# Kernel tuning notes

Measured on AMD Instinct MI355X. Metric: run time of the kernel, lower is better.

The kernel has to match this reference:

```python
import jax, jax.numpy as jnp
import numpy as np
import math

B, S, HID, H = 2, 1024, 768, 12
D = HID // H  # 64
ALPHA = 32.0


def setup_inputs() -> dict:
    key = jax.random.key(0)
    ks = jax.random.split(key, 8)
    return {
        "hidden_states": jax.random.normal(ks[0], (B, S, HID), jnp.float32),
        "attention_mask": jnp.zeros((B, 1, 1, S), jnp.float32),
        "head_mask": jnp.ones((1, H, 1, 1), jnp.float32),
        "rel_pos": jax.random.normal(ks[1], (B, H, S, S), jnp.float32),
        "rel_2d_pos": jax.random.normal(ks[2], (B, H, S, S), jnp.float32),
        "Wq": jax.random.normal(ks[3], (HID, HID), jnp.float32) * 0.02,
        "bq": jnp.zeros((HID,), jnp.float32),
        "Wk": jax.random.normal(ks[4], (HID, HID), jnp.float32) * 0.02,
        "bk": jnp.zeros((HID,), jnp.float32),
        "Wv": jax.random.normal(ks[5], (HID, HID), jnp.float32) * 0.02,
        "bv": jnp.zeros((HID,), jnp.float32),
    }


def _heads(x):
    # [B,S,HID] -> [B,H,S,D]
    return x.reshape(B, S, H, D).transpose(0, 2, 1, 3)


def cogview_softmax(scores, alpha=ALPHA):
    s = scores / alpha
    m = jnp.max(s, axis=-1, keepdims=True)
    return jax.nn.softmax((s - m) * alpha, axis=-1)


def reference(hidden_states, attention_mask, head_mask, rel_pos, rel_2d_pos,
              Wq, bq, Wk, bk, Wv, bv):
    norm = math.sqrt(D)
    q = _heads(hidden_states @ Wq + bq) / norm   # [B,H,S,D]
    k = _heads(hidden_states @ Wk + bk)
    v = _heads(hidden_states @ Wv + bv)
    scores = jnp.einsum("bhsd,bhtd->bhst", q, k)
    scores = scores + (rel_pos + rel_2d_pos) / norm
    scores = scores + attention_mask
    probs = cogview_softmax(scores)              # [B,H,S,S]
    probs = probs * head_mask
    ctx = jnp.einsum("bhst,bhtd->bhsd", probs, v)
    ctx = ctx.transpose(0, 2, 1, 3).reshape(B, S, HID)
    return ctx
```

## Files before the change

kernel.cpp:

```cpp
#include <hip/hip_runtime.h>
#include <hip/hip_bf16.h>
#include <cstdint>

#define BB   2
#define SS   1024
#define HIDD 768
#define NH   12
#define DH   64
#define BH   (BB*NH)

typedef short bf16x8 __attribute__((ext_vector_type(8)));
typedef float f32x4  __attribute__((ext_vector_type(4)));

__device__ __forceinline__ unsigned short f2b(float x) {
    union { float f; uint32_t u; } v; v.f = x;
    uint32_t u = v.u;
    uint32_t r = (u + 0x7fffu + ((u >> 16) & 1u)) >> 16;
    return (unsigned short)r;
}

__device__ __forceinline__ void async16(const void* g, void* l) {
    __builtin_amdgcn_global_load_lds(
        (const __attribute__((address_space(1))) unsigned int*)g,
        (__attribute__((address_space(3))) unsigned int*)l,
        16, 0, 0);
}

__global__ void cvt_x(const float* __restrict__ x, unsigned short* __restrict__ xb) {
    int i = blockIdx.x * blockDim.x + threadIdx.x;
    float4 v = ((const float4*)x)[i];
    ushort4 o;
    o.x = f2b(v.x); o.y = f2b(v.y); o.z = f2b(v.z); o.w = f2b(v.w);
    ((ushort4*)xb)[i] = o;
}

__global__ void transpose_w(const float* __restrict__ Wq, const float* __restrict__ Wk,
                            const float* __restrict__ Wv, unsigned short* __restrict__ Wt) {
    __shared__ float tile[32][33];
    const int w = blockIdx.z;
    const float* W = (w == 0) ? Wq : (w == 1) ? Wk : Wv;
    const int tx = threadIdx.x & 31, ty = threadIdx.x >> 5;
    const int k0 = blockIdx.x * 32, n0 = blockIdx.y * 32;
    for (int p = 0; p < 4; ++p)
        tile[ty + p * 8][tx] = W[(k0 + ty + p * 8) * HIDD + n0 + tx];
    __syncthreads();
    for (int p = 0; p < 4; ++p) {
        int n = n0 + ty + p * 8;
        Wt[(w * HIDD + n) * HIDD + k0 + tx] = f2b(tile[tx][ty + p * 8]);
    }
}

__global__ __launch_bounds__(256) void qkv_gemm(
    const unsigned short* __restrict__ Xb, const unsigned short* __restrict__ Wt,
    const float* __restrict__ bq, const float* __restrict__ bk, const float* __restrict__ bv,
    unsigned short* __restrict__ Qh, unsigned short* __restrict__ Kh,
    unsigned short* __restrict__ Vh) {
    __shared__ __align__(16) unsigned short lA[2][128 * 32];
    __shared__ __align__(16) unsigned short lB[2][64 * 32];
    const int t = threadIdx.x;
    const int wave = t >> 6, lane = t & 63;
    const int l15 = lane & 15, quad = lane >> 4;
    const int m0 = blockIdx.x * 128;
    const int n0 = blockIdx.y * 64;
    const int wm = wave * 32;

    f32x4 acc[2][4] = {};

    auto stage = [&](int k0, int b) {
        #pragma unroll
        for (int r = 0; r < 2; ++r) {
            int ci = r * 256 + t;
            async16(Xb + (m0 + (ci >> 2)) * HIDD + k0 + (ci & 3) * 8,
                    &lA[b][(r * 256 + wave * 64) * 8]);
        }
        async16(Wt + (n0 + (t >> 2)) * HIDD + k0 + (t & 3) * 8,
                &lB[b][(wave * 64) * 8]);
    };

    stage(0, 0);
    for (int ki = 0; ki < 24; ++ki) {
        const int cur = ki & 1;
        __syncthreads();
        if (ki < 23) stage((ki + 1) * 32, cur ^ 1);
        bf16x8 af[2], bf[4];
        #pragma unroll
        for (int i = 0; i < 2; ++i)
            af[i] = *(const bf16x8*)&lA[cur][(wm + i * 16 + l15) * 32 + quad * 8];
        #pragma unroll
        for (int j = 0; j < 4; ++j)
            bf[j] = *(const bf16x8*)&lB[cur][(j * 16 + l15) * 32 + quad * 8];
        #pragma unroll
        for (int i = 0; i < 2; ++i)
            #pragma unroll
            for (int j = 0; j < 4; ++j)
                acc[i][j] = __builtin_amdgcn_mfma_f32_16x16x32_bf16(af[i], bf[j], acc[i][j], 0, 0, 0);
    }

    const int sect = (n0 >= 1536) ? 2 : (n0 >= 768) ? 1 : 0;
    const float* bias = (sect == 0) ? bq : (sect == 1) ? bk : bv;
    unsigned short* dst = (sect == 0) ? Qh : (sect == 1) ? Kh : Vh;
    const float scale = (sect == 0) ? 0.125f : 1.0f;
    #pragma unroll
    for (int i = 0; i < 2; ++i) {
        #pragma unroll
        for (int j = 0; j < 4; ++j) {
            int n  = n0 + j * 16 + l15;
            int nn = n - sect * HIDD;
            int h = nn >> 6, d = nn & 63;
            float bval = bias[nn];
            #pragma unroll
            for (int r = 0; r < 4; ++r) {
                int m = m0 + wm + i * 16 + quad * 4 + r;
                int b = m >> 10, s = m & 1023;
                float v = (acc[i][j][r] + bval) * scale;
                dst[((size_t)(b * NH + h) * SS + s) * DH + d] = f2b(v);
            }
        }
    }
}

__global__ __launch_bounds__(256) void transpose_v(
    const unsigned short* __restrict__ Vh, unsigned short* __restrict__ VhT) {
    __shared__ unsigned short tile[64][65];
    const int t = threadIdx.x;
    const int bh = blockIdx.y;
    const int s0 = blockIdx.x * 64;
    const int tx = t & 63, ty = t >> 6;
    const unsigned short* src = Vh + (size_t)bh * SS * DH;
    #pragma unroll
    for (int p = 0; p < 16; ++p)
        tile[ty + p * 4][tx] = src[(size_t)(s0 + ty + p * 4) * DH + tx];
    __syncthreads();
    unsigned short* dst = VhT + (size_t)bh * DH * SS;
    #pragma unroll
    for (int p = 0; p < 16; ++p)
        dst[(size_t)(ty + p * 4) * SS + s0 + tx] = tile[tx][ty + p * 4];
}

__global__ __launch_bounds__(256, 2) void flash_attn(
    const unsigned short* __restrict__ Qh, const unsigned short* __restrict__ Kh,
    const unsigned short* __restrict__ VhT,
    const float* __restrict__ rel, const float* __restrict__ rel2d,
    const float* __restrict__ amask, const float* __restrict__ hmask,
    float* __restrict__ out) {
    __shared__ __align__(16) char smemraw[17408];
    float* o_l = (float*)smemraw;
    float* m_l = (float*)(smemraw + 16384);
    float* l_l = (float*)(smemraw + 16640);

    const int t = threadIdx.x;
    const int wave = t >> 6, lane = t & 63;
    const int l15 = lane & 15, quad = lane >> 4;
    const int bh = blockIdx.y;
    const int b = bh / NH, h = bh % NH;
    const int m0 = blockIdx.x * 16;

    const unsigned short* Qp = Qh + (size_t)bh * SS * DH;
    const unsigned short* Kp = Kh + (size_t)bh * SS * DH;
    const unsigned short* Vp = VhT + (size_t)bh * DH * SS;
    const float* relp  = rel   + (size_t)bh * SS * SS;
    const float* rel2p = rel2d + (size_t)bh * SS * SS;
    const float* maskp = amask + (size_t)b * SS;

    unsigned short* Pw = (unsigned short*)smemraw + wave * (16 * 72);

    const int jbeg = wave * 256;

    bf16x8 qf0 = *(const bf16x8*)&Qp[(m0 + l15) * DH + quad * 8];
    bf16x8 qf1 = *(const bf16x8*)&Qp[(m0 + l15) * DH + 32 + quad * 8];

    float mk_all[16];
    #pragma unroll
    for (int tc = 0; tc < 16; ++tc)
        mk_all[tc] = maskp[jbeg + (tc >> 2) * 64 + (tc & 3) * 16 + l15];

    f32x4 o[4] = {};
    float mrow[4] = {-1e30f, -1e30f, -1e30f, -1e30f};
    float lrow[4] = {0.f, 0.f, 0.f, 0.f};

    float ra[16], rb[16];
    bf16x8 k0f[4], k1f[4];

    #define LOAD_BIAS(J0)                                                      \
        _Pragma("unroll")                                                      \
        for (int c = 0; c < 4; ++c)                                            \
            _Pragma("unroll")                                                  \
            for (int r = 0; r < 4; ++r) {                                      \
                size_t idx = (size_t)(m0 + quad * 4 + r) * SS + (J0) + c * 16 + l15; \
                ra[c * 4 + r] = relp[idx];                                     \
                rb[c * 4 + r] = rel2p[idx];                                    \
            }
    #define LOAD_K(J0)                                                         \
        _Pragma("unroll")                                                      \
        for (int c = 0; c < 4; ++c) {                                          \
            k0f[c] = *(const bf16x8*)&Kp[((J0) + c * 16 + l15) * DH + quad * 8];      \
            k1f[c] = *(const bf16x8*)&Kp[((J0) + c * 16 + l15) * DH + 32 + quad * 8]; \
        }

    LOAD_BIAS(jbeg)
    LOAD_K(jbeg)

    #pragma unroll
    for (int tt = 0; tt < 4; ++tt) {
        const int j0 = jbeg + tt * 64;
        bf16x8 v0f[4], v1f[4];
        #pragma unroll
        for (int dt = 0; dt < 4; ++dt) {
            v0f[dt] = *(const bf16x8*)&Vp[(dt * 16 + l15) * SS + j0 + quad * 8];
            v1f[dt] = *(const bf16x8*)&Vp[(dt * 16 + l15) * SS + j0 + 32 + quad * 8];
        }
        f32x4 sc[4] = {};
        #pragma unroll
        for (int c = 0; c < 4; ++c) {
            sc[c] = __builtin_amdgcn_mfma_f32_16x16x32_bf16(qf0, k0f[c], sc[c], 0, 0, 0);
            sc[c] = __builtin_amdgcn_mfma_f32_16x16x32_bf16(qf1, k1f[c], sc[c], 0, 0, 0);
        }
        float sv[4][4];
        #pragma unroll
        for (int c = 0; c < 4; ++c)
            #pragma unroll
            for (int r = 0; r < 4; ++r)
                sv[c][r] = sc[c][r] + (ra[c * 4 + r] + rb[c * 4 + r]) * 0.125f
                         + mk_all[tt * 4 + c];
        if (tt < 3) {
            LOAD_BIAS(j0 + 64)
            LOAD_K(j0 + 64)
        }
        float alpha[4];
        #pragma unroll
        for (int r = 0; r < 4; ++r) {
            float mx = fmaxf(fmaxf(sv[0][r], sv[1][r]), fmaxf(sv[2][r], sv[3][r]));
            #pragma unroll
            for (int off = 1; off < 16; off <<= 1) mx = fmaxf(mx, __shfl_xor(mx, off, 64));
            float mnew = fmaxf(mrow[r], mx);
            alpha[r] = __expf(mrow[r] - mnew);
            mrow[r] = mnew;
            float rs = 0.f;
            #pragma unroll
            for (int c = 0; c < 4; ++c) {
                float p = __expf(sv[c][r] - mnew);
                sv[c][r] = p;
                rs += p;
            }
            #pragma unroll
            for (int off = 1; off < 16; off <<= 1) rs += __shfl_xor(rs, off, 64);
            lrow[r] = lrow[r] * alpha[r] + rs;
            o[0][r] *= alpha[r]; o[1][r] *= alpha[r]; o[2][r] *= alpha[r]; o[3][r] *= alpha[r];
        }
        #pragma unroll
        for (int c = 0; c < 4; ++c)
            #pragma unroll
            for (int r = 0; r < 4; ++r)
                Pw[(quad * 4 + r) * 72 + c * 16 + l15] = f2b(sv[c][r]);

        bf16x8 pf0 = *(const bf16x8*)&Pw[l15 * 72 + quad * 8];
        bf16x8 pf1 = *(const bf16x8*)&Pw[l15 * 72 + 32 + quad * 8];
        #pragma unroll
        for (int dt = 0; dt < 4; ++dt) {
            o[dt] = __builtin_amdgcn_mfma_f32_16x16x32_bf16(pf0, v0f[dt], o[dt], 0, 0, 0);
            o[dt] = __builtin_amdgcn_mfma_f32_16x16x32_bf16(pf1, v1f[dt], o[dt], 0, 0, 0);
        }
    }
    #undef LOAD_BIAS
    #undef LOAD_K

    __syncthreads();
    #pragma unroll
    for (int dt = 0; dt < 4; ++dt)
        #pragma unroll
        for (int r = 0; r < 4; ++r)
            o_l[(wave * 16 + quad * 4 + r) * 64 + dt * 16 + l15] = o[dt][r];
    if (l15 == 0) {
        #pragma unroll
        for (int r = 0; r < 4; ++r) {
            m_l[wave * 16 + quad * 4 + r] = mrow[r];
            l_l[wave * 16 + quad * 4 + r] = lrow[r];
        }
    }
    __syncthreads();

    const float hm = hmask[h];
    const int col = t & 63, rsel = t >> 6;
    #pragma unroll
    for (int rr = 0; rr < 4; ++rr) {
        int row = rsel * 4 + rr;
        float m01 = fmaxf(m_l[row], m_l[16 + row]);
        float m23 = fmaxf(m_l[32 + row], m_l[48 + row]);
        float mt = fmaxf(m01, m23);
        float lt = 0.f, val = 0.f;
        #pragma unroll
        for (int w = 0; w < 4; ++w) {
            float sc = __expf(m_l[w * 16 + row] - mt);
            lt += sc * l_l[w * 16 + row];
            val += sc * o_l[(w * 16 + row) * 64 + col];
        }
        int s = m0 + row;
        out[((size_t)(b * SS + s)) * HIDD + h * DH + col] = val * hm / lt;
    }
}

extern "C" void kernel_launch(void* const* d_in, const int* in_sizes, int n_in,
                              void* d_out, int out_size, void* d_ws, size_t ws_size,
                              hipStream_t stream) {
    const float* hs    = (const float*)d_in[0];
    const float* am    = (const float*)d_in[1];
    const float* hm    = (const float*)d_in[2];
    const float* rel   = (const float*)d_in[3];
    const float* rel2d = (const float*)d_in[4];
    const float* Wq    = (const float*)d_in[5];
    const float* bq    = (const float*)d_in[6];
    const float* Wk    = (const float*)d_in[7];
    const float* bk    = (const float*)d_in[8];
    const float* Wv    = (const float*)d_in[9];
    const float* bv    = (const float*)d_in[10];
    float* out = (float*)d_out;

    unsigned short* Xb  = (unsigned short*)d_ws;
    unsigned short* Wt  = Xb + 2048 * HIDD;
    unsigned short* Qh  = Wt + 3 * HIDD * HIDD;
    unsigned short* Kh  = Qh + (size_t)BH * SS * DH;
    unsigned short* Vh  = Kh + (size_t)BH * SS * DH;
    unsigned short* VhT = Vh + (size_t)BH * SS * DH;

    cvt_x<<<(2048 * HIDD / 4) / 256, 256, 0, stream>>>(hs, Xb);
    dim3 gT(24, 24, 3);
    transpose_w<<<gT, 256, 0, stream>>>(Wq, Wk, Wv, Wt);
    dim3 gG(16, 36);
    qkv_gemm<<<gG, 256, 0, stream>>>(Xb, Wt, bq, bk, bv, Qh, Kh, Vh);
    dim3 gV(16, BH);
    transpose_v<<<gV, 256, 0, stream>>>(Vh, VhT);
    dim3 gF(64, BH);
    flash_attn<<<gF, 256, 0, stream>>>(Qh, Kh, VhT, rel, rel2d, am, hm, out);
}
```

Baseline: 296.6 us.

## Stage relative-position bias through LDS with async global loads

Replaces the per-lane scalar register loads of rel_pos and rel_2d_pos, previously prefetched one tile ahead, with global_load_lds async copies into a per-wave LDS staging buffer. The rows are then read back from LDS in the MFMA fragment layout. The aim is wide 16-byte coalesced transfers and lower register pressure, and launch bounds rise to 3 blocks per SU to raise occupancy. The cost is losing the cross-iteration prefetch: each iteration waits on vmcnt(0) before use, and LDS per block grows to about 41KB.

```diff
diff --git a/kernel.cpp b/kernel.cpp
--- a/kernel.cpp
+++ b/kernel.cpp
@@ -137,16 +137,13 @@
         dst[(size_t)(ty + p * 4) * SS + s0 + tx] = tile[tx][ty + p * 4];
 }
 
-__global__ __launch_bounds__(256, 2) void flash_attn(
+__global__ __launch_bounds__(256, 3) void flash_attn(
     const unsigned short* __restrict__ Qh, const unsigned short* __restrict__ Kh,
     const unsigned short* __restrict__ VhT,
     const float* __restrict__ rel, const float* __restrict__ rel2d,
     const float* __restrict__ amask, const float* __restrict__ hmask,
     float* __restrict__ out) {
-    __shared__ __align__(16) char smemraw[17408];
-    float* o_l = (float*)smemraw;
-    float* m_l = (float*)(smemraw + 16384);
-    float* l_l = (float*)(smemraw + 16640);
+    __shared__ __align__(16) char smemraw[41984];
 
     const int t = threadIdx.x;
     const int wave = t >> 6, lane = t & 63;
@@ -162,7 +159,9 @@
     const float* rel2p = rel2d + (size_t)bh * SS * SS;
     const float* maskp = amask + (size_t)b * SS;
 
-    unsigned short* Pw = (unsigned short*)smemraw + wave * (16 * 72);
+    float* stgA = (float*)(smemraw + wave * 8192);
+    float* stgB = stgA + 1024;
+    unsigned short* Pw = (unsigned short*)(smemraw + 32768) + wave * (16 * 72);
 
     const int jbeg = wave * 256;
 
@@ -178,54 +177,47 @@
     float mrow[4] = {-1e30f, -1e30f, -1e30f, -1e30f};
     float lrow[4] = {0.f, 0.f, 0.f, 0.f};
 
-    float ra[16], rb[16];
-    bf16x8 k0f[4], k1f[4];
-
-    #define LOAD_BIAS(J0)                                                      \
-        _Pragma("unroll")                                                      \
-        for (int c = 0; c < 4; ++c)                                            \
-            _Pragma("unroll")                                                  \
-            for (int r = 0; r < 4; ++r) {                                      \
-                size_t idx = (size_t)(m0 + quad * 4 + r) * SS + (J0) + c * 16 + l15; \
-                ra[c * 4 + r] = relp[idx];                                     \
-                rb[c * 4 + r] = rel2p[idx];                                    \
-            }
-    #define LOAD_K(J0)                                                         \
-        _Pragma("unroll")                                                      \
-        for (int c = 0; c < 4; ++c) {                                          \
-            k0f[c] = *(const bf16x8*)&Kp[((J0) + c * 16 + l15) * DH + quad * 8];      \
-            k1f[c] = *(const bf16x8*)&Kp[((J0) + c * 16 + l15) * DH + 32 + quad * 8]; \
-        }
-
-    LOAD_BIAS(jbeg)
-    LOAD_K(jbeg)
-
-    #pragma unroll
     for (int tt = 0; tt < 4; ++tt) {
         const int j0 = jbeg + tt * 64;
+
+        #pragma unroll
+        for (int i = 0; i < 4; ++i) {
+            const float* gA = relp  + (size_t)(m0 + 4 * i + quad) * SS + j0 + l15 * 4;
+            const float* gB = rel2p + (size_t)(m0 + 4 * i + quad) * SS + j0 + l15 * 4;
+            async16(gA, stgA + i * 256);
+            async16(gB, stgB + i * 256);
+        }
+        bf16x8 k0f[4], k1f[4];
+        #pragma unroll
+        for (int c = 0; c < 4; ++c) {
+            k0f[c] = *(const bf16x8*)&Kp[(j0 + c * 16 + l15) * DH + quad * 8];
+            k1f[c] = *(const bf16x8*)&Kp[(j0 + c * 16 + l15) * DH + 32 + quad * 8];
+        }
         bf16x8 v0f[4], v1f[4];
         #pragma unroll
         for (int dt = 0; dt < 4; ++dt) {
             v0f[dt] = *(const bf16x8*)&Vp[(dt * 16 + l15) * SS + j0 + quad * 8];
             v1f[dt] = *(const bf16x8*)&Vp[(dt * 16 + l15) * SS + j0 + 32 + quad * 8];
         }
+
         f32x4 sc[4] = {};
         #pragma unroll
         for (int c = 0; c < 4; ++c) {
             sc[c] = __builtin_amdgcn_mfma_f32_16x16x32_bf16(qf0, k0f[c], sc[c], 0, 0, 0);
             sc[c] = __builtin_amdgcn_mfma_f32_16x16x32_bf16(qf1, k1f[c], sc[c], 0, 0, 0);
         }
+
+        asm volatile("s_waitcnt vmcnt(0)" ::: "memory");
+
         float sv[4][4];
         #pragma unroll
         for (int c = 0; c < 4; ++c)
             #pragma unroll
-            for (int r = 0; r < 4; ++r)
-                sv[c][r] = sc[c][r] + (ra[c * 4 + r] + rb[c * 4 + r]) * 0.125f
-                         + mk_all[tt * 4 + c];
-        if (tt < 3) {
-            LOAD_BIAS(j0 + 64)
-            LOAD_K(j0 + 64)
-        }
+            for (int r = 0; r < 4; ++r) {
+                int fi = (quad * 4 + r) * 64 + c * 16 + l15;
+                sv[c][r] = sc[c][r] + (stgA[fi] + stgB[fi]) * 0.125f + mk_all[tt * 4 + c];
+            }
+
         float alpha[4];
         #pragma unroll
         for (int r = 0; r < 4; ++r) {
@@ -261,10 +253,11 @@
             o[dt] = __builtin_amdgcn_mfma_f32_16x16x32_bf16(pf1, v1f[dt], o[dt], 0, 0, 0);
         }
     }
-    #undef LOAD_BIAS
-    #undef LOAD_K
 
     __syncthreads();
+    float* o_l = (float*)smemraw;
+    float* m_l = (float*)(smemraw + 16384);
+    float* l_l = (float*)(smemraw + 16640);
     #pragma unroll
     for (int dt = 0; dt < 4; ++dt)
         #pragma unroll
```

Result: no change. 291.9 us (-1.6%).
